# Optimization experiments

Hardware: AMD Instinct MI355X
Metric: run time of the kernel (lower is better)

The kernel has to match this reference:

```python
import jax, jax.numpy as jnp
import numpy as np

B, TK, NK, H = 64, 512, 256, 512

def _masked_renorm_softmax(scores, mask):
    # softmax over last dim, multiply by mask, renormalize (as in the torch code)
    p = jax.nn.softmax(scores, axis=-1) * mask
    return p / jnp.sum(p, axis=-1, keepdims=True)

def setup_inputs() -> dict:
    key = jax.random.key(0)
    ks = jax.random.split(key, 14)
    s = 0.02
    return {
        "s_t_hat": jax.random.normal(ks[0], (B, 2 * H), jnp.float32),
        "encoder_outputs_token": jax.random.normal(ks[1], (B, TK, H), jnp.float32),
        "encoder_outputs_node": jax.random.normal(ks[2], (B, NK, H), jnp.float32),
        "node_to_token": jax.random.randint(ks[3], (B, TK), 0, NK),
        "enc_padding_mask_token": jnp.ones((B, TK), jnp.float32),
        "enc_padding_mask_node": jnp.ones((B, NK), jnp.float32),
        "graph": jax.random.uniform(ks[4], (B, NK, NK), jnp.float32),
        "flow": jax.random.uniform(ks[5], (B, NK), jnp.float32),
        # parameters (Linear weights stored as [in, out]; x @ W == torch Linear)
        "W_c": jax.random.normal(ks[6], (H,), jnp.float32) * s,          # Linear(1, H)
        "W_tok": jax.random.normal(ks[7], (H, H), jnp.float32) * s,      # encode_proj_token
        "W_node": jax.random.normal(ks[8], (H, H), jnp.float32) * s,     # encode_proj_node
        "W_dec": jax.random.normal(ks[9], (2 * H, H), jnp.float32) * s,  # decode_proj
        "b_dec": jnp.zeros((H,), jnp.float32),
        "v_tok": jax.random.normal(ks[10], (H,), jnp.float32) * s,       # v_token
        "v_node": jax.random.normal(ks[11], (H,), jnp.float32) * s,      # v_node
    }

def reference(s_t_hat, encoder_outputs_token, encoder_outputs_node, node_to_token,
              enc_padding_mask_token, enc_padding_mask_node, graph, flow,
              W_c, W_tok, W_node, W_dec, b_dec, v_tok, v_node):
    # projections
    enc_tok_feat = jnp.einsum('bth,hk->btk', encoder_outputs_token, W_tok)   # [B,TK,H]
    enc_node_feat = jnp.einsum('bnh,hk->bnk', encoder_outputs_node, W_node)  # [B,NK,H]
    dec_fea = s_t_hat @ W_dec + b_dec                                        # [B,H]
    flow_feat = flow[..., None] * W_c                                        # [B,NK,H]

    # node attention
    e_node = jnp.tanh(enc_node_feat + dec_fea[:, None, :] + flow_feat)
    scores_node = jnp.einsum('bnh,h->bn', e_node, v_node)                    # [B,NK]
    attn_dist_node = _masked_renorm_softmax(scores_node, enc_padding_mask_node)

    # gather node attention onto tokens via node_to_token indices
    gathered = jnp.take_along_axis(attn_dist_node, node_to_token, axis=1)    # [B,TK]
    attn_dist_node_to_token = _masked_renorm_softmax(gathered, enc_padding_mask_token)

    # token attention
    e_tok = jnp.tanh(enc_tok_feat + dec_fea[:, None, :])
    scores_tok = jnp.einsum('bth,h->bt', e_tok, v_tok)                       # [B,TK]
    attn_dist_token = _masked_renorm_softmax(scores_tok, enc_padding_mask_token)

    # mix and context
    final_attn = 0.5 * attn_dist_token + 0.5 * attn_dist_node_to_token      # [B,TK]
    c_t = jnp.einsum('bt,bth->bh', final_attn, encoder_outputs_token)        # [B,H]

    # multi-hop graph diffusion of node attention
    zero_hop = attn_dist_node                                                # [B,NK]
    one_hop = jnp.einsum('bn,bnm->bm', zero_hop, graph)
    two_hop = jnp.einsum('bn,bnm->bm', one_hop, graph)
    flow_out = (zero_hop + one_hop + two_hop) * 0.33333

    return (c_t, final_attn, attn_dist_node, flow_out)
```

## Files before the change

kernel.cpp:

```cpp
#include <hip/hip_runtime.h>
#include <math.h>

constexpr int kB = 64;
constexpr int kTK = 512;
constexpr int kNK = 256;
constexpr int kH = 512;
constexpr int kTokBlocks = kB * kTK / 64;
constexpr int kNodeBlocks = kB * kNK / 64;

typedef float f32x4 __attribute__((ext_vector_type(4)));
typedef __bf16 bf16x8 __attribute__((ext_vector_type(8)));

__device__ __forceinline__ unsigned short f32_to_bf16(float f) {
  return (unsigned short)((__float_as_uint(f) + 0x8000u) >> 16);
}

__device__ __forceinline__ unsigned pk_bf16x2(float lo, float hi) {
  return (unsigned)f32_to_bf16(lo) | ((unsigned)f32_to_bf16(hi) << 16);
}

__device__ __forceinline__ float tanh_fast(float x) {
  float e = __builtin_amdgcn_exp2f(x * 2.8853900817779268f);
  return 1.0f - 2.0f * __builtin_amdgcn_rcpf(e + 1.0f);
}

__device__ __forceinline__ void gload_lds16(const void* g, void* l) {
  __builtin_amdgcn_global_load_lds(
      (__attribute__((address_space(1))) void*)(g),
      (__attribute__((address_space(3))) void*)(l), 16, 0, 0);
}

__global__ __launch_bounds__(256) void prep_kernel(
    const float* __restrict__ Wtok, const float* __restrict__ Wnode,
    unsigned short* __restrict__ WtokT, unsigned short* __restrict__ WnodeT,
    const float* __restrict__ s_t_hat, const float* __restrict__ W_dec,
    float* __restrict__ dec_part) {
  __shared__ float sm[32 * 33];
  const int tid = threadIdx.x;
  if (blockIdx.x < 512) {
    const int idx = blockIdx.x;
    const int z = idx >> 8, rem = idx & 255;
    const int bx = rem & 15, by = rem >> 4;
    const float* W = z ? Wnode : Wtok;
    unsigned short* T = z ? WnodeT : WtokT;
    const int tx = tid & 31, ty = tid >> 5;
#pragma unroll
    for (int i = 0; i < 4; ++i)
      sm[(ty + 8 * i) * 33 + tx] =
          W[(size_t)(by * 32 + ty + 8 * i) * kH + bx * 32 + tx];
    __syncthreads();
#pragma unroll
    for (int i = 0; i < 4; ++i)
      T[(size_t)(bx * 32 + ty + 8 * i) * kH + by * 32 + tx] =
          f32_to_bf16(sm[tx * 33 + ty + 8 * i]);
  } else {
    const int r = blockIdx.x - 512;
    const int b = r >> 3, s = r & 7;
    if (tid < 128) sm[tid] = s_t_hat[(size_t)b * 1024 + s * 128 + tid];
    __syncthreads();
    float a0 = 0.f, a1 = 0.f;
    const float* w = W_dec + (size_t)(s * 128) * kH;
#pragma unroll 8
    for (int k = 0; k < 128; ++k) {
      a0 = fmaf(sm[k], w[(size_t)k * kH + tid], a0);
      a1 = fmaf(sm[k], w[(size_t)k * kH + tid + 256], a1);
    }
    dec_part[(size_t)(b * 8 + s) * kH + tid] = a0;
    dec_part[(size_t)(b * 8 + s) * kH + tid + 256] = a1;
  }
}

__global__ __launch_bounds__(512, 4) void scores_fused_kernel(
    const float* __restrict__ enc_tok, const float* __restrict__ enc_node,
    const unsigned short* __restrict__ WtokT,
    const unsigned short* __restrict__ WnodeT,
    const float* __restrict__ dec_part, const float* __restrict__ b_dec,
    const float* __restrict__ flow, const float* __restrict__ W_c,
    const float* __restrict__ v_tok, const float* __restrict__ v_node,
    float* __restrict__ scores_tok, float* __restrict__ scores_node) {
  const int tid = threadIdx.x;
  const int wave = tid >> 6, lane = tid & 63;
  const int quad = lane >> 4, l15 = lane & 15;
  const bool is_node = blockIdx.x >= kTokBlocks;
  const int bidx = is_node ? (int)blockIdx.x - kTokBlocks : (int)blockIdx.x;
  const float* A = is_node ? enc_node : enc_tok;
  const unsigned short* WT = is_node ? WnodeT : WtokT;
  const float* v = is_node ? v_node : v_tok;
  float* scores = is_node ? scores_node : scores_tok;
  const int ROWS = is_node ? kNK : kTK;
  const int b = is_node ? (bidx >> 2) : (bidx >> 3);
  const int row0 = (is_node ? (bidx & 3) : (bidx & 7)) * 64;

  __shared__ __align__(16) float As32[2][4096];
  __shared__ float red[8][64];

  const f32x4 fzero = {0.f, 0.f, 0.f, 0.f};
  f32x4 acc[4][4];
#pragma unroll
  for (int i = 0; i < 4; ++i)
#pragma unroll
    for (int j = 0; j < 4; ++j) acc[i][j] = fzero;

  const int lrow0 = wave * 4 + (lane >> 4);
  const int gseg0 = (lane & 15) ^ (lrow0 & 7);
  const int lrow1 = 32 + lrow0;
  const int gseg1 = (lane & 15) ^ (lrow1 & 7);
  const float* asrc0 = A + (size_t)(b * ROWS + row0 + lrow0) * kH + gseg0 * 4;
  const float* asrc1 = A + (size_t)(b * ROWS + row0 + lrow1) * kH + gseg1 * 4;
  auto stage = [&](int kc, int buf) {
    gload_lds16(asrc0 + kc * 64, &As32[buf][(wave * 4) * 64]);
    gload_lds16(asrc1 + kc * 64, &As32[buf][(32 + wave * 4) * 64]);
  };

  auto readfrag = [&](int buf, int khalf, int mi) {
    const int row = mi * 16 + l15;
    const int rw = row & 7;
    const int q2 = khalf * 8 + quad * 2;
    const f32x4 a = *(const f32x4*)&As32[buf][row * 64 + ((q2 ^ rw) << 2)];
    const f32x4 c = *(const f32x4*)&As32[buf][row * 64 + (((q2 + 1) ^ rw) << 2)];
    union { bf16x8 v; unsigned u[4]; } t;
    t.u[0] = pk_bf16x2(a[0], a[1]);
    t.u[1] = pk_bf16x2(a[2], a[3]);
    t.u[2] = pk_bf16x2(c[0], c[1]);
    t.u[3] = pk_bf16x2(c[2], c[3]);
    return t.v;
  };

  const int n0 = wave * 64;
  const unsigned short* bbase = WT + (size_t)(n0 + l15) * kH + quad * 8;
  bf16x8 bbuf[2][2];
  auto loadB = [&](int sb, int g, int half) {
    bbuf[sb][0] = *(const bf16x8*)(bbase + (size_t)(16 * (2 * half + 0)) * kH + g * 32);
    bbuf[sb][1] = *(const bf16x8*)(bbase + (size_t)(16 * (2 * half + 1)) * kH + g * 32);
  };

  stage(0, 0);
  loadB(0, 0, 0);
  loadB(1, 0, 1);
  __syncthreads();

#pragma unroll
  for (int kc = 0; kc < 8; ++kc) {
    if (kc < 7) stage(kc + 1, (kc + 1) & 1);
#pragma unroll
    for (int khalf = 0; khalf < 2; ++khalf) {
      const int g = kc * 2 + khalf;
      bf16x8 afr[4];
#pragma unroll
      for (int mi = 0; mi < 4; ++mi) afr[mi] = readfrag(kc & 1, khalf, mi);
      if (g > 0) loadB(1, g, 1);
      __builtin_amdgcn_s_setprio(1);
#pragma unroll
      for (int mi = 0; mi < 4; ++mi)
#pragma unroll
        for (int ni = 0; ni < 2; ++ni)
          acc[mi][ni] = __builtin_amdgcn_mfma_f32_16x16x32_bf16(
              afr[mi], bbuf[0][ni], acc[mi][ni], 0, 0, 0);
      __builtin_amdgcn_s_setprio(0);
      if (g < 15) loadB(0, g + 1, 0);
      __builtin_amdgcn_s_setprio(1);
#pragma unroll
      for (int mi = 0; mi < 4; ++mi)
#pragma unroll
        for (int ni = 0; ni < 2; ++ni)
          acc[mi][ni + 2] = __builtin_amdgcn_mfma_f32_16x16x32_bf16(
              afr[mi], bbuf[1][ni], acc[mi][ni + 2], 0, 0, 0);
      __builtin_amdgcn_s_setprio(0);
    }
    __syncthreads();
  }

  float dec2[4], vv2[4], wc2[4];
#pragma unroll
  for (int ni = 0; ni < 4; ++ni) {
    const int col = n0 + 16 * ni + l15;
    float d = b_dec[col];
#pragma unroll
    for (int p = 0; p < 8; ++p) d += dec_part[(size_t)(b * 8 + p) * kH + col];
    dec2[ni] = d;
    vv2[ni] = v[col];
    wc2[ni] = is_node ? W_c[col] : 0.f;
  }
#pragma unroll
  for (int mi = 0; mi < 4; ++mi) {
#pragma unroll
    for (int reg = 0; reg < 4; ++reg) {
      const int row = 16 * mi + quad * 4 + reg;
      const float fl = is_node ? flow[b * kNK + row0 + row] : 0.f;
      float p = 0.f;
#pragma unroll
      for (int ni = 0; ni < 4; ++ni)
        p += tanh_fast(fmaf(fl, wc2[ni], acc[mi][ni][reg] + dec2[ni])) * vv2[ni];
#pragma unroll
      for (int off = 1; off < 16; off <<= 1) p += __shfl_xor(p, off, 64);
      if (l15 == 0) red[wave][row] = p;
    }
  }
  __syncthreads();
  if (tid < 64) {
    float s = 0.f;
#pragma unroll
    for (int w = 0; w < 8; ++w) s += red[w][tid];
    scores[b * ROWS + row0 + tid] = s;
  }
}

__device__ __forceinline__ float block_sum_512(float v, float* rbuf) {
#pragma unroll
  for (int off = 32; off >= 1; off >>= 1) v += __shfl_xor(v, off, 64);
  if ((threadIdx.x & 63) == 0) rbuf[threadIdx.x >> 6] = v;
  __syncthreads();
  float s = rbuf[0];
#pragma unroll
  for (int w = 1; w < 8; ++w) s += rbuf[w];
  __syncthreads();
  return s;
}

__global__ __launch_bounds__(512) void softmax_mix_kernel(
    const float* __restrict__ scores_node, const float* __restrict__ scores_tok,
    const int* __restrict__ node_to_token,
    const float* __restrict__ mask_tok, const float* __restrict__ mask_node,
    float* __restrict__ out_final, float* __restrict__ out_attn_node,
    float* __restrict__ out_flow) {
  const int b = blockIdx.x, tid = threadIdx.x;
  __shared__ float an_sh[kNK];
  __shared__ float rbuf[8];

  if (tid < kNK) out_flow[b * kNK + tid] = 0.f;

  float en = 0.f;
  if (tid < kNK)
    en = expf(scores_node[b * kNK + tid]) * mask_node[b * kNK + tid];
  float sn = block_sum_512(en, rbuf);
  float an = en / sn;
  if (tid < kNK) {
    an_sh[tid] = an;
    out_attn_node[b * kNK + tid] = an;
  }
  __syncthreads();

  const float mt = mask_tok[b * kTK + tid];
  const int idx = node_to_token[b * kTK + tid];
  float eg = expf(an_sh[idx]) * mt;
  float sg = block_sum_512(eg, rbuf);
  float an2t = eg / sg;

  float et = expf(scores_tok[b * kTK + tid]) * mt;
  float st = block_sum_512(et, rbuf);
  float at = et / st;

  out_final[b * kTK + tid] = 0.5f * (at + an2t);
}

__global__ __launch_bounds__(512) void ct_flow1_kernel(
    const float* __restrict__ final_attn, const float* __restrict__ enc_tok,
    const float* __restrict__ attn_node, const float* __restrict__ graph,
    float* __restrict__ ctp, float* __restrict__ fp1) {
  const int tid = threadIdx.x;
  if (blockIdx.x < 512) {
    const int b = blockIdx.x >> 3, s = blockIdx.x & 7;
    __shared__ float fa[64];
    __shared__ float part[4][512];
    if (tid < 64) fa[tid] = final_attn[b * kTK + s * 64 + tid];
    __syncthreads();
    const int h4 = (tid & 127) * 4, tsub = tid >> 7;
    float4 acc = {0.f, 0.f, 0.f, 0.f};
    const float* base =
        enc_tok + ((size_t)(b * kTK + s * 64 + tsub * 16)) * kH + h4;
#pragma unroll
    for (int t = 0; t < 16; ++t) {
      float4 e = *(const float4*)(base + (size_t)t * kH);
      const float w = fa[tsub * 16 + t];
      acc.x = fmaf(w, e.x, acc.x); acc.y = fmaf(w, e.y, acc.y);
      acc.z = fmaf(w, e.z, acc.z); acc.w = fmaf(w, e.w, acc.w);
    }
    *(float4*)&part[tsub][h4] = acc;
    __syncthreads();
    if (tid < 128) {
      float4 s0 = {0.f, 0.f, 0.f, 0.f};
#pragma unroll
      for (int p = 0; p < 4; ++p) {
        float4 pp = *(const float4*)&part[p][tid * 4];
        s0.x += pp.x; s0.y += pp.y; s0.z += pp.z; s0.w += pp.w;
      }
      *(float4*)&ctp[((size_t)(b * 8 + s)) * kH + tid * 4] = s0;
    }
  } else {
    const int rr = blockIdx.x - 512;
    const int b = rr >> 2, sl = rr & 3;
    __shared__ float z[64];
    __shared__ float part[8][256];
    if (tid < 64) z[tid] = attn_node[b * kNK + sl * 64 + tid];
    __syncthreads();
    const int m4 = (tid & 63) * 4, nsub = tid >> 6;
    float4 acc = {0.f, 0.f, 0.f, 0.f};
    const float* g =
        graph + ((size_t)(b * kNK + sl * 64 + nsub * 8)) * kNK + m4;
#pragma unroll
    for (int n = 0; n < 8; ++n) {
      float4 gg = *(const float4*)(g + (size_t)n * kNK);
      const float w = z[nsub * 8 + n];
      acc.x = fmaf(w, gg.x, acc.x); acc.y = fmaf(w, gg.y, acc.y);
      acc.z = fmaf(w, gg.z, acc.z); acc.w = fmaf(w, gg.w, acc.w);
    }
    *(float4*)&part[nsub][m4] = acc;
    __syncthreads();
    if (tid < 64) {
      float4 s0 = {0.f, 0.f, 0.f, 0.f};
#pragma unroll
      for (int p = 0; p < 8; ++p) {
        float4 pp = *(const float4*)&part[p][tid * 4];
        s0.x += pp.x; s0.y += pp.y; s0.z += pp.z; s0.w += pp.w;
      }
      *(float4*)&fp1[((size_t)(b * 4 + sl)) * kNK + tid * 4] = s0;
    }
  }
}

__global__ __launch_bounds__(512) void ct_flow2_kernel(
    const float* __restrict__ ctp, const float* __restrict__ fp1,
    const float* __restrict__ attn_node, const float* __restrict__ graph,
    float* __restrict__ out_ct, float* __restrict__ out_flow) {
  const int tid = threadIdx.x;
  if (blockIdx.x < 64) {
    const int b = blockIdx.x;
    __shared__ float acc_sh[4][512];
    const int h4 = (tid & 127) * 4, part = tid >> 7;
    float4 a = {0.f, 0.f, 0.f, 0.f};
#pragma unroll
    for (int j = 0; j < 2; ++j) {
      float4 c = *(const float4*)&ctp[((size_t)(b * 8 + part * 2 + j)) * kH + h4];
      a.x += c.x; a.y += c.y; a.z += c.z; a.w += c.w;
    }
    *(float4*)&acc_sh[part][h4] = a;
    __syncthreads();
    if (tid < 128) {
      float4 s = {0.f, 0.f, 0.f, 0.f};
#pragma unroll
      for (int p = 0; p < 4; ++p) {
        float4 pp = *(const float4*)&acc_sh[p][tid * 4];
        s.x += pp.x; s.y += pp.y; s.z += pp.z; s.w += pp.w;
      }
      *(float4*)&out_ct[b * kH + tid * 4] = s;
    }
  } else {
    const int rr = blockIdx.x - 64;
    const int b = rr >> 2, sl = rr & 3;
    __shared__ float one_sh[64];
    __shared__ float part2[8][256];
    if (tid < 64) {
      const int n = sl * 64 + tid;
      float one = 0.f;
#pragma unroll
      for (int p = 0; p < 4; ++p) one += fp1[((size_t)(b * 4 + p)) * kNK + n];
      one_sh[tid] = one;
      atomicAdd(&out_flow[b * kNK + n],
                (attn_node[b * kNK + n] + one) * 0.33333f);
    }
    __syncthreads();
    const int m4 = (tid & 63) * 4, nsub = tid >> 6;
    float4 acc = {0.f, 0.f, 0.f, 0.f};
    const float* g =
        graph + ((size_t)(b * kNK + sl * 64 + nsub * 8)) * kNK + m4;
#pragma unroll
    for (int n = 0; n < 8; ++n) {
      float4 gg = *(const float4*)(g + (size_t)n * kNK);
      const float w = one_sh[sl * 0 + nsub * 8 + n];
      acc.x = fmaf(w, gg.x, acc.x); acc.y = fmaf(w, gg.y, acc.y);
      acc.z = fmaf(w, gg.z, acc.z); acc.w = fmaf(w, gg.w, acc.w);
    }
    *(float4*)&part2[nsub][m4] = acc;
    __syncthreads();
    if (tid < 64) {
      float4 s = {0.f, 0.f, 0.f, 0.f};
#pragma unroll
      for (int p = 0; p < 8; ++p) {
        float4 pp = *(const float4*)&part2[p][tid * 4];
        s.x += pp.x; s.y += pp.y; s.z += pp.z; s.w += pp.w;
      }
      float* dst = &out_flow[b * kNK + tid * 4];
      atomicAdd(dst + 0, s.x * 0.33333f);
      atomicAdd(dst + 1, s.y * 0.33333f);
      atomicAdd(dst + 2, s.z * 0.33333f);
      atomicAdd(dst + 3, s.w * 0.33333f);
    }
  }
}

extern "C" void kernel_launch(void* const* d_in, const int* in_sizes, int n_in,
                              void* d_out, int out_size, void* d_ws, size_t ws_size,
                              hipStream_t stream) {
  (void)in_sizes; (void)n_in; (void)out_size; (void)ws_size;
  const float* s_t_hat  = (const float*)d_in[0];
  const float* enc_tok  = (const float*)d_in[1];
  const float* enc_node = (const float*)d_in[2];
  const int*   n2t      = (const int*)d_in[3];
  const float* mask_tok = (const float*)d_in[4];
  const float* mask_nd  = (const float*)d_in[5];
  const float* graph    = (const float*)d_in[6];
  const float* flow     = (const float*)d_in[7];
  const float* W_c      = (const float*)d_in[8];
  const float* W_tok    = (const float*)d_in[9];
  const float* W_node   = (const float*)d_in[10];
  const float* W_dec    = (const float*)d_in[11];
  const float* b_dec    = (const float*)d_in[12];
  const float* v_tok    = (const float*)d_in[13];
  const float* v_node   = (const float*)d_in[14];

  float* out = (float*)d_out;
  float* out_ct        = out;
  float* out_final     = out + kB * kH;
  float* out_attn_node = out + 2 * kB * kH;
  float* out_flow      = out_attn_node + kB * kNK;

  float* ws = (float*)d_ws;
  float* scores_tok  = ws;
  float* scores_node = ws + 32768;
  float* dec_part    = ws + 49152;
  float* ctp         = dec_part;
  float* fp1         = ws + 311296;
  unsigned short* WtokT  = (unsigned short*)(ws + 376832);
  unsigned short* WnodeT = WtokT + kH * kH;

  prep_kernel<<<1024, 256, 0, stream>>>(W_tok, W_node, WtokT, WnodeT,
                                        s_t_hat, W_dec, dec_part);
  scores_fused_kernel<<<kTokBlocks + kNodeBlocks, 512, 0, stream>>>(
      enc_tok, enc_node, WtokT, WnodeT, dec_part, b_dec, flow, W_c,
      v_tok, v_node, scores_tok, scores_node);
  softmax_mix_kernel<<<kB, 512, 0, stream>>>(scores_node, scores_tok, n2t,
                                             mask_tok, mask_nd, out_final,
                                             out_attn_node, out_flow);
  ct_flow1_kernel<<<768, 512, 0, stream>>>(out_final, enc_tok, out_attn_node,
                                           graph, ctp, fp1);
  ct_flow2_kernel<<<320, 512, 0, stream>>>(ctp, fp1, out_attn_node, graph,
                                           out_ct, out_flow);
}
```

Baseline: 228.0 us.

## Convert A tile to bf16 once in LDS instead of per-wave fragment conversion

Each K-chunk of the fp32 A tile is now converted cooperatively by all threads into a swizzled bf16 LDS buffer. MFMA fragments are then read as one bf16x8 load instead of two fp32x4 loads plus packing in every wave. This removes the redundant fp32-to-bf16 conversion that every wave repeated on the same rows, and halves LDS read traffic for fragments. In exchange it adds an extra LDS write pass and a second LDS buffer. It also uses a manual waitcnt that waits on all vector memory loads, which may stall on in-flight B loads.

After: 235.9 us. +3.4%, slower.

```diff
diff --git a/kernel.cpp b/kernel.cpp
--- a/kernel.cpp
+++ b/kernel.cpp
@@ -15,13 +15,14 @@
   return (unsigned short)((__float_as_uint(f) + 0x8000u) >> 16);
 }
 
-__device__ __forceinline__ unsigned pk_bf16x2(float lo, float hi) {
-  return (unsigned)f32_to_bf16(lo) | ((unsigned)f32_to_bf16(hi) << 16);
-}
-
 __device__ __forceinline__ float tanh_fast(float x) {
   float e = __builtin_amdgcn_exp2f(x * 2.8853900817779268f);
   return 1.0f - 2.0f * __builtin_amdgcn_rcpf(e + 1.0f);
+}
+
+__device__ __forceinline__ void lds_barrier() {
+  __builtin_amdgcn_s_waitcnt(0xC07F);
+  __builtin_amdgcn_s_barrier();
 }
 
 __device__ __forceinline__ void gload_lds16(const void* g, void* l) {
@@ -91,7 +92,8 @@
   const int b = is_node ? (bidx >> 2) : (bidx >> 3);
   const int row0 = (is_node ? (bidx & 3) : (bidx & 7)) * 64;
 
-  __shared__ __align__(16) float As32[2][4096];
+  __shared__ __align__(16) float fbuf[2][4096];
+  __shared__ __align__(16) unsigned short hbuf[2][4096];
   __shared__ float red[8][64];
 
   const f32x4 fzero = {0.f, 0.f, 0.f, 0.f};
@@ -101,29 +103,31 @@
 #pragma unroll
     for (int j = 0; j < 4; ++j) acc[i][j] = fzero;
 
-  const int lrow0 = wave * 4 + (lane >> 4);
-  const int gseg0 = (lane & 15) ^ (lrow0 & 7);
-  const int lrow1 = 32 + lrow0;
-  const int gseg1 = (lane & 15) ^ (lrow1 & 7);
-  const float* asrc0 = A + (size_t)(b * ROWS + row0 + lrow0) * kH + gseg0 * 4;
-  const float* asrc1 = A + (size_t)(b * ROWS + row0 + lrow1) * kH + gseg1 * 4;
+  const float* asrcw =
+      A + (size_t)(b * ROWS + row0 + wave * 8 + (lane >> 4)) * kH + (lane & 15) * 4;
   auto stage = [&](int kc, int buf) {
-    gload_lds16(asrc0 + kc * 64, &As32[buf][(wave * 4) * 64]);
-    gload_lds16(asrc1 + kc * 64, &As32[buf][(32 + wave * 4) * 64]);
+    gload_lds16(asrcw + kc * 64, &fbuf[buf][(wave * 8) * 64]);
+    gload_lds16(asrcw + 4 * kH + kc * 64, &fbuf[buf][(wave * 8 + 4) * 64]);
   };
 
-  auto readfrag = [&](int buf, int khalf, int mi) {
+  auto cvt = [&](int buf) {
+#pragma unroll
+    for (int j = 0; j < 2; ++j) {
+      const int e0 = j * 2048 + tid * 4;
+      const int row = e0 >> 6, k = e0 & 63;
+      const f32x4 x = *(const f32x4*)&fbuf[buf][e0];
+      ushort4 h;
+      h.x = f32_to_bf16(x[0]); h.y = f32_to_bf16(x[1]);
+      h.z = f32_to_bf16(x[2]); h.w = f32_to_bf16(x[3]);
+      const int s16 = (k >> 3) ^ (row & 7);
+      *(ushort4*)((char*)&hbuf[buf][0] + row * 128 + s16 * 16 + (k & 7) * 2) = h;
+    }
+  };
+
+  auto readfrag = [&](int buf, int ks, int mi) {
     const int row = mi * 16 + l15;
-    const int rw = row & 7;
-    const int q2 = khalf * 8 + quad * 2;
-    const f32x4 a = *(const f32x4*)&As32[buf][row * 64 + ((q2 ^ rw) << 2)];
-    const f32x4 c = *(const f32x4*)&As32[buf][row * 64 + (((q2 + 1) ^ rw) << 2)];
-    union { bf16x8 v; unsigned u[4]; } t;
-    t.u[0] = pk_bf16x2(a[0], a[1]);
-    t.u[1] = pk_bf16x2(a[2], a[3]);
-    t.u[2] = pk_bf16x2(c[0], c[1]);
-    t.u[3] = pk_bf16x2(c[2], c[3]);
-    return t.v;
+    const int s16 = (ks * 4 + quad) ^ (row & 7);
+    return *(const bf16x8*)((const char*)&hbuf[buf][0] + row * 128 + s16 * 16);
   };
 
   const int n0 = wave * 64;
@@ -137,17 +141,20 @@
   stage(0, 0);
   loadB(0, 0, 0);
   loadB(1, 0, 1);
-  __syncthreads();
 
 #pragma unroll
   for (int kc = 0; kc < 8; ++kc) {
+    __builtin_amdgcn_s_waitcnt(0x0F70);
+    __builtin_amdgcn_sched_barrier(0);
+    cvt(kc & 1);
     if (kc < 7) stage(kc + 1, (kc + 1) & 1);
-#pragma unroll
-    for (int khalf = 0; khalf < 2; ++khalf) {
-      const int g = kc * 2 + khalf;
+    lds_barrier();
+#pragma unroll
+    for (int ks = 0; ks < 2; ++ks) {
+      const int g = kc * 2 + ks;
       bf16x8 afr[4];
 #pragma unroll
-      for (int mi = 0; mi < 4; ++mi) afr[mi] = readfrag(kc & 1, khalf, mi);
+      for (int mi = 0; mi < 4; ++mi) afr[mi] = readfrag(kc & 1, ks, mi);
       if (g > 0) loadB(1, g, 1);
       __builtin_amdgcn_s_setprio(1);
 #pragma unroll
@@ -167,7 +174,6 @@
               afr[mi], bbuf[1][ni], acc[mi][ni + 2], 0, 0, 0);
       __builtin_amdgcn_s_setprio(0);
     }
-    __syncthreads();
   }
 
   float dec2[4], vv2[4], wc2[4];
```
